# Performance work log

Hardware: AMD Instinct MI355X
Metric: run time of the kernel (lower is better)

The kernel has to match this reference:

```python
import jax, jax.numpy as jnp
import numpy as np


def _maxpool2(x):
    # 2x2 max pool, stride 2, valid padding (H, W even). x: [B,H,W,C]
    B, H, W, C = x.shape
    return x.reshape(B, H // 2, 2, W // 2, 2, C).max(axis=(2, 4))


def setup_inputs() -> dict:
    key = jax.random.key(0)
    ks = jax.random.split(key, 9)
    B, H, W, C = 8, 64, 64, 512
    cfg, ch = C // 8, C // 2
    std = 0.02
    return {
        "x": jax.random.normal(ks[0], (B, H, W, C), jnp.float32),
        "theta_w": jax.random.normal(ks[1], (C, cfg), jnp.float32) * std,
        "theta_b": jnp.zeros((cfg,), jnp.float32),
        "phi_w": jax.random.normal(ks[2], (C, cfg), jnp.float32) * std,
        "phi_b": jnp.zeros((cfg,), jnp.float32),
        "g_w": jax.random.normal(ks[3], (C, ch), jnp.float32) * std,
        "g_b": jnp.zeros((ch,), jnp.float32),
        "o3_w": jax.random.normal(ks[4], (ch, C), jnp.float32) * std,
        "o3_b": jnp.zeros((C,), jnp.float32),
        # original initializes gamma to 0; use 0.1 so the attention branch contributes
        "gamma": jnp.full((1,), 0.1, jnp.float32),
    }


def reference(x, theta_w, theta_b, phi_w, phi_b, g_w, g_b, o3_w, o3_b, gamma):
    B, H, W, C = x.shape
    cfg = theta_w.shape[1]
    ch = g_w.shape[1]
    hw = H * W
    hwd = (H // 2) * (W // 2)

    theta = jnp.einsum("bhwc,cf->bhwf", x, theta_w) + theta_b          # [B,H,W,cfg]
    phi = _maxpool2(jnp.einsum("bhwc,cf->bhwf", x, phi_w) + phi_b)     # [B,H/2,W/2,cfg]
    g = _maxpool2(jnp.einsum("bhwc,cg->bhwg", x, g_w) + g_b)           # [B,H/2,W/2,ch]

    theta_f = theta.reshape(B, hw, cfg)
    phi_f = phi.reshape(B, hwd, cfg)
    g_f = g.reshape(B, hwd, ch)

    # s[b,i,j] = phi[b,i] . theta[b,j]; softmax over j (last axis, Keras default)
    s = jnp.einsum("bif,bjf->bij", phi_f, theta_f)                     # [B,hwd,hw]
    beta = jax.nn.softmax(s, axis=-1)
    # o = matmul(beta, g, transpose_a=True): o[b,j,c] = sum_i beta[b,i,j] g[b,i,c]
    o = jnp.einsum("bij,bic->bjc", beta, g_f)                          # [B,hw,ch]
    o = o.reshape(B, H, W, ch)
    o = jnp.einsum("bhwg,gc->bhwc", o, o3_w) + o3_b                    # [B,H,W,C]
    return gamma * o + x
```

## Files before the change

### kernel.cpp

```cpp
#include <hip/hip_runtime.h>
#include <cstdint>

typedef short short8 __attribute__((ext_vector_type(8)));
typedef float floatx4 __attribute__((ext_vector_type(4)));

__device__ __forceinline__ unsigned short f2bf(float f) {
    unsigned int u = __builtin_bit_cast(unsigned int, f);
    u += 0x7FFFu + ((u >> 16) & 1u);
    return (unsigned short)(u >> 16);
}
__device__ __forceinline__ float bf2f(unsigned short h) {
    unsigned int u = ((unsigned int)h) << 16;
    return __builtin_bit_cast(float, u);
}

__device__ __forceinline__ void async_copy16(const void* g, void* lds) {
    __builtin_amdgcn_global_load_lds(
        (const __attribute__((address_space(1))) void*)g,
        (__attribute__((address_space(3))) void*)lds, 16, 0, 0);
}

template<int EPI>
__global__ __launch_bounds__(256) void mfma_gemm(
    const unsigned short* __restrict__ A, const unsigned short* __restrict__ B,
    void* __restrict__ Cout, const float* __restrict__ bias,
    const float* __restrict__ gamma, const float* __restrict__ resid,
    float* __restrict__ lbuf,
    int lda, int ldb, int ldc, int K,
    long long sA, long long sB, long long sC)
{
    __shared__ unsigned short As[4096];
    __shared__ unsigned short Bs[4096];

    const int tid = threadIdx.x;
    const int wv = tid >> 6, ln = tid & 63;
    const int r16 = ln & 15, q8 = ln >> 4;
    const int wm = (wv >> 1) * 64, wn = (wv & 1) * 64;
    const int m0 = blockIdx.y * 128, n0 = blockIdx.x * 128;
    const int zb = blockIdx.z;

    const unsigned short* Ag = A + (long long)zb * sA;
    const unsigned short* Bg = B + (long long)zb * sB;

    floatx4 acc[4][4] = {};

    for (int k0 = 0; k0 < K; k0 += 32) {
        #pragma unroll
        for (int q = 0; q < 2; ++q) {
            int chunk = wv * 2 + q;
            int e = (chunk << 9) + ln * 8;
            int row = e >> 5, col = e & 31;
            async_copy16(Ag + (size_t)(m0 + row) * lda + (k0 + col), &As[chunk << 9]);
            async_copy16(Bg + (size_t)(n0 + row) * ldb + (k0 + col), &Bs[chunk << 9]);
        }
        __syncthreads();

        short8 af[4], bff[4];
        #pragma unroll
        for (int i = 0; i < 4; ++i) {
            af[i]  = *(const short8*)&As[(wm + i * 16 + r16) * 32 + q8 * 8];
            bff[i] = *(const short8*)&Bs[(wn + i * 16 + r16) * 32 + q8 * 8];
        }
        #pragma unroll
        for (int mi = 0; mi < 4; ++mi)
            #pragma unroll
            for (int ni = 0; ni < 4; ++ni)
                acc[mi][ni] = __builtin_amdgcn_mfma_f32_16x16x32_bf16(
                    af[mi], bff[ni], acc[mi][ni], 0, 0, 0);
        __syncthreads();
    }

    if (EPI == 2) {
        float* C = (float*)Cout;
        const float gm = gamma[0];
        #pragma unroll
        for (int ni = 0; ni < 4; ++ni) {
            const int n = n0 + wn + ni * 16 + r16;
            const float bs = bias[n];
            #pragma unroll
            for (int mi = 0; mi < 4; ++mi)
                #pragma unroll
                for (int r = 0; r < 4; ++r) {
                    int m = m0 + wm + mi * 16 + q8 * 4 + r;
                    C[(size_t)m * ldc + n] = gm * (acc[mi][ni][r] + bs) + resid[(size_t)m * ldc + n];
                }
        }
    } else {
        unsigned short* C = (unsigned short*)Cout + (long long)zb * sC;
        float colsum[4] = {0.f, 0.f, 0.f, 0.f};
        #pragma unroll
        for (int ni = 0; ni < 4; ++ni) {
            const int n = n0 + wn + ni * 16 + r16;
            const float bs = (EPI == 1) ? bias[n] : 0.f;
            #pragma unroll
            for (int mi = 0; mi < 4; ++mi)
                #pragma unroll
                for (int r = 0; r < 4; ++r) {
                    int m = m0 + wm + mi * 16 + q8 * 4 + r;
                    float v = acc[mi][ni][r];
                    if (EPI == 1) v += bs;
                    if (EPI == 3) { v = __expf(v - 20.f); colsum[ni] += v; }
                    C[(size_t)m * ldc + n] = f2bf(v);
                }
        }
        if (EPI == 3) {
            #pragma unroll
            for (int ni = 0; ni < 4; ++ni) {
                float s = colsum[ni];
                s += __shfl_xor(s, 16);
                s += __shfl_xor(s, 32);
                if (q8 == 0)
                    atomicAdd(&lbuf[zb * 1024 + n0 + wn + ni * 16 + r16], s);
            }
        }
    }
}

__global__ __launch_bounds__(256) void prep_w_kernel(
    const float* __restrict__ theta_w, const float* __restrict__ phi_w,
    const float* __restrict__ g_w, const float* __restrict__ o3_w,
    const float* __restrict__ theta_b, const float* __restrict__ phi_b,
    unsigned short* __restrict__ tpwT, unsigned short* __restrict__ gwT,
    unsigned short* __restrict__ o3wT, float* __restrict__ biasTP,
    float* __restrict__ lbuf)
{
    int t = blockIdx.x * 256 + threadIdx.x;
    if (t < 65536) {
        int n = t >> 9, k = t & 511;
        float v = (n < 64) ? theta_w[k * 64 + n] : phi_w[k * 64 + (n - 64)];
        tpwT[t] = f2bf(v);
    } else if (t < 196608) {
        int e = t - 65536; int n = e >> 9, k = e & 511;
        gwT[e] = f2bf(g_w[k * 256 + n]);
    } else if (t < 327680) {
        int e = t - 196608; int n = e >> 8, k = e & 255;
        o3wT[e] = f2bf(o3_w[k * 512 + n]);
    } else if (t < 327808) {
        int j = t - 327680;
        biasTP[j] = (j < 64) ? theta_b[j] : phi_b[j - 64];
    } else if (t < 336000) {
        lbuf[t - 327808] = 0.f;
    }
}

__global__ __launch_bounds__(256) void cast_x_kernel(
    const float* __restrict__ x, unsigned short* __restrict__ xb)
{
    size_t t = (size_t)blockIdx.x * 256 + threadIdx.x;
    float4 v = ((const float4*)x)[t];
    ushort4 h;
    h.x = f2bf(v.x); h.y = f2bf(v.y); h.z = f2bf(v.z); h.w = f2bf(v.w);
    ((ushort4*)xb)[t] = h;
}

__global__ __launch_bounds__(256) void maxpool_phi_kernel(
    const unsigned short* __restrict__ tpF, unsigned short* __restrict__ phiP)
{
    int t = blockIdx.x * 256 + threadIdx.x;
    int f = t & 63, i = (t >> 6) & 1023, b = t >> 16;
    int ph = i >> 5, pw = i & 31;
    size_t base = ((size_t)(b * 64 + 2 * ph) * 64 + 2 * pw) * 128 + 64 + f;
    float v0 = bf2f(tpF[base]),        v1 = bf2f(tpF[base + 128]);
    float v2 = bf2f(tpF[base + 8192]), v3 = bf2f(tpF[base + 8192 + 128]);
    phiP[t] = f2bf(fmaxf(fmaxf(v0, v1), fmaxf(v2, v3)));
}

__global__ __launch_bounds__(256) void maxpoolT_g_kernel(
    const unsigned short* __restrict__ gF, unsigned short* __restrict__ gPT)
{
    __shared__ unsigned short tile[16][256];
    int b = blockIdx.y, i0 = blockIdx.x * 16, c = threadIdx.x;
    #pragma unroll
    for (int il = 0; il < 16; ++il) {
        int i = i0 + il, ph = i >> 5, pw = i & 31;
        size_t base = ((size_t)(b * 64 + 2 * ph) * 64 + 2 * pw) * 256 + c;
        float v0 = bf2f(gF[base]),         v1 = bf2f(gF[base + 256]);
        float v2 = bf2f(gF[base + 16384]), v3 = bf2f(gF[base + 16384 + 256]);
        tile[il][c] = f2bf(fmaxf(fmaxf(v0, v1), fmaxf(v2, v3)));
    }
    __syncthreads();
    unsigned short* dst = gPT + ((size_t)(b * 256 + c) * 1024 + i0);
    short8 v0, v1;
    #pragma unroll
    for (int il = 0; il < 8; ++il) { v0[il] = (short)tile[il][c]; v1[il] = (short)tile[il + 8][c]; }
    *(short8*)dst = v0;
    *(short8*)(dst + 8) = v1;
}

__global__ __launch_bounds__(256) void scale_gpt_kernel(
    unsigned short* __restrict__ gPT, const float* __restrict__ lbuf)
{
    int t = blockIdx.x * 256 + threadIdx.x;
    int i = t & 1023, b = t >> 18;
    float rl = 1.0f / lbuf[b * 1024 + i];
    gPT[t] = f2bf(bf2f(gPT[t]) * rl);
}

extern "C" void kernel_launch(void* const* d_in, const int* in_sizes, int n_in,
                              void* d_out, int out_size, void* d_ws, size_t ws_size,
                              hipStream_t stream)
{
    const float* x       = (const float*)d_in[0];
    const float* theta_w = (const float*)d_in[1];
    const float* theta_b = (const float*)d_in[2];
    const float* phi_w   = (const float*)d_in[3];
    const float* phi_b   = (const float*)d_in[4];
    const float* g_w     = (const float*)d_in[5];
    const float* g_b     = (const float*)d_in[6];
    const float* o3_w    = (const float*)d_in[7];
    const float* o3_b    = (const float*)d_in[8];
    const float* gamma   = (const float*)d_in[9];

    char* ws = (char*)d_ws;
    const size_t MB = 1u << 20;
    unsigned short* tpwT = (unsigned short*)(ws);
    unsigned short* gwT  = (unsigned short*)(ws + 131072);
    unsigned short* o3wT = (unsigned short*)(ws + 393216);
    float* biasTP        = (float*)(ws + 655360);
    float* lbuf          = (float*)(ws + 655872);
    unsigned short* gPT  = (unsigned short*)(ws + 1 * MB);
    unsigned short* tpF  = (unsigned short*)(ws + 5 * MB);
    unsigned short* phiP = (unsigned short*)(ws + 13 * MB);
    unsigned short* gF   = (unsigned short*)(ws + 14 * MB);
    unsigned short* xb   = (unsigned short*)(ws + 30 * MB);
    unsigned short* o_   = (unsigned short*)(ws + 30 * MB);
    unsigned short* sT   = (unsigned short*)d_out;

    prep_w_kernel<<<1313, 256, 0, stream>>>(theta_w, phi_w, g_w, o3_w, theta_b, phi_b,
                                            tpwT, gwT, o3wT, biasTP, lbuf);
    cast_x_kernel<<<16384, 256, 0, stream>>>(x, xb);
    mfma_gemm<1><<<dim3(2, 256, 1), 256, 0, stream>>>(
        xb, gwT, gF, g_b, nullptr, nullptr, nullptr, 512, 512, 256, 512, 0, 0, 0);
    maxpoolT_g_kernel<<<dim3(64, 8), 256, 0, stream>>>(gF, gPT);
    mfma_gemm<1><<<dim3(1, 256, 1), 256, 0, stream>>>(
        xb, tpwT, tpF, biasTP, nullptr, nullptr, nullptr, 512, 512, 128, 512, 0, 0, 0);
    maxpool_phi_kernel<<<2048, 256, 0, stream>>>(tpF, phiP);
    mfma_gemm<3><<<dim3(8, 32, 8), 256, 0, stream>>>(
        tpF, phiP, sT, nullptr, nullptr, nullptr, lbuf,
        128, 64, 1024, 64, 4096LL * 128, 1024LL * 64, 4096LL * 1024);
    scale_gpt_kernel<<<8192, 256, 0, stream>>>(gPT, lbuf);
    mfma_gemm<0><<<dim3(2, 32, 8), 256, 0, stream>>>(
        sT, gPT, o_, nullptr, nullptr, nullptr, nullptr,
        1024, 1024, 256, 1024, 4096LL * 1024, 256LL * 1024, 4096LL * 256);
    mfma_gemm<2><<<dim3(4, 256, 1), 256, 0, stream>>>(
        o_, o3wT, d_out, o3_b, gamma, x, nullptr, 256, 256, 512, 256, 0, 0, 0);
}
```

Measured before the change: 267.4 us.

## Fuse attention score/softmax/PV into one kernel and merge projection GEMMs

Merges the theta/phi/g projections into one GEMM that reads fp32 x directly and converts it to bf16 in-kernel, which removes the separate cast pass. The score GEMM now only accumulates softmax denominators and no longer writes the 4096x1024 score matrix. A new fused kernel recomputes scores per tile, applies exp and normalization, and multiplies by pooled g in LDS. This avoids the large sT round trip through HBM and the scale_gpt pass, at the cost of computing the score GEMM twice and running a fused kernel with heavier LDS use and no async copies.

```diff
diff --git a/kernel.cpp b/kernel.cpp
--- a/kernel.cpp
+++ b/kernel.cpp
@@ -20,9 +20,9 @@
         (__attribute__((address_space(3))) void*)lds, 16, 0, 0);
 }
 
-template<int EPI>
+template<bool AFP32, int EPI>
 __global__ __launch_bounds__(256) void mfma_gemm(
-    const unsigned short* __restrict__ A, const unsigned short* __restrict__ B,
+    const void* __restrict__ Avoid, const unsigned short* __restrict__ B,
     void* __restrict__ Cout, const float* __restrict__ bias,
     const float* __restrict__ gamma, const float* __restrict__ resid,
     float* __restrict__ lbuf,
@@ -39,19 +39,39 @@
     const int m0 = blockIdx.y * 128, n0 = blockIdx.x * 128;
     const int zb = blockIdx.z;
 
-    const unsigned short* Ag = A + (long long)zb * sA;
     const unsigned short* Bg = B + (long long)zb * sB;
 
     floatx4 acc[4][4] = {};
 
     for (int k0 = 0; k0 < K; k0 += 32) {
-        #pragma unroll
-        for (int q = 0; q < 2; ++q) {
-            int chunk = wv * 2 + q;
-            int e = (chunk << 9) + ln * 8;
-            int row = e >> 5, col = e & 31;
-            async_copy16(Ag + (size_t)(m0 + row) * lda + (k0 + col), &As[chunk << 9]);
-            async_copy16(Bg + (size_t)(n0 + row) * ldb + (k0 + col), &Bs[chunk << 9]);
+        if (AFP32) {
+            const float* Af = (const float*)Avoid;
+            #pragma unroll
+            for (int p = 0; p < 4; ++p) {
+                int u = p * 256 + tid;
+                int row = u >> 3, c4 = u & 7;
+                float4 v = *(const float4*)(Af + (size_t)(m0 + row) * lda + k0 + c4 * 4);
+                ushort4 h;
+                h.x = f2bf(v.x); h.y = f2bf(v.y); h.z = f2bf(v.z); h.w = f2bf(v.w);
+                *(ushort4*)&As[row * 32 + c4 * 4] = h;
+            }
+            #pragma unroll
+            for (int q = 0; q < 2; ++q) {
+                int chunk = wv * 2 + q;
+                int e = (chunk << 9) + ln * 8;
+                int row = e >> 5, col = e & 31;
+                async_copy16(Bg + (size_t)(n0 + row) * ldb + (k0 + col), &Bs[chunk << 9]);
+            }
+        } else {
+            const unsigned short* Ag = (const unsigned short*)Avoid + (long long)zb * sA;
+            #pragma unroll
+            for (int q = 0; q < 2; ++q) {
+                int chunk = wv * 2 + q;
+                int e = (chunk << 9) + ln * 8;
+                int row = e >> 5, col = e & 31;
+                async_copy16(Ag + (size_t)(m0 + row) * lda + (k0 + col), &As[chunk << 9]);
+                async_copy16(Bg + (size_t)(n0 + row) * ldb + (k0 + col), &Bs[chunk << 9]);
+            }
         }
         __syncthreads();
 
@@ -85,97 +105,204 @@
                     C[(size_t)m * ldc + n] = gm * (acc[mi][ni][r] + bs) + resid[(size_t)m * ldc + n];
                 }
         }
+    } else if (EPI == 4) {
+        float colsum[4] = {0.f, 0.f, 0.f, 0.f};
+        #pragma unroll
+        for (int ni = 0; ni < 4; ++ni)
+            #pragma unroll
+            for (int mi = 0; mi < 4; ++mi)
+                #pragma unroll
+                for (int r = 0; r < 4; ++r)
+                    colsum[ni] += __expf(acc[mi][ni][r] - 20.f);
+        #pragma unroll
+        for (int ni = 0; ni < 4; ++ni) {
+            float s = colsum[ni];
+            s += __shfl_xor(s, 16);
+            s += __shfl_xor(s, 32);
+            if (q8 == 0)
+                atomicAdd(&lbuf[zb * 1024 + n0 + wn + ni * 16 + r16], s);
+        }
     } else {
         unsigned short* C = (unsigned short*)Cout + (long long)zb * sC;
-        float colsum[4] = {0.f, 0.f, 0.f, 0.f};
         #pragma unroll
         for (int ni = 0; ni < 4; ++ni) {
             const int n = n0 + wn + ni * 16 + r16;
-            const float bs = (EPI == 1) ? bias[n] : 0.f;
+            const float bs = bias[n];
             #pragma unroll
             for (int mi = 0; mi < 4; ++mi)
                 #pragma unroll
                 for (int r = 0; r < 4; ++r) {
                     int m = m0 + wm + mi * 16 + q8 * 4 + r;
-                    float v = acc[mi][ni][r];
-                    if (EPI == 1) v += bs;
-                    if (EPI == 3) { v = __expf(v - 20.f); colsum[ni] += v; }
-                    C[(size_t)m * ldc + n] = f2bf(v);
+                    C[(size_t)m * ldc + n] = f2bf(acc[mi][ni][r] + bs);
                 }
         }
-        if (EPI == 3) {
-            #pragma unroll
-            for (int ni = 0; ni < 4; ++ni) {
-                float s = colsum[ni];
-                s += __shfl_xor(s, 16);
-                s += __shfl_xor(s, 32);
-                if (q8 == 0)
-                    atomicAdd(&lbuf[zb * 1024 + n0 + wn + ni * 16 + r16], s);
+    }
+}
+
+__global__ __launch_bounds__(256) void attn_fused_kernel(
+    const unsigned short* __restrict__ tpgF,
+    const unsigned short* __restrict__ phiP,
+    const unsigned short* __restrict__ gPT,
+    const float* __restrict__ lbuf,
+    unsigned short* __restrict__ o_)
+{
+    __shared__ unsigned short th_s[128 * 72];
+    __shared__ unsigned short ph_s[64 * 72];
+    __shared__ unsigned short es[128 * 72];
+    __shared__ unsigned short gs[128 * 72];
+    __shared__ float rl_s[1024];
+
+    const int tid = threadIdx.x, wv = tid >> 6, ln = tid & 63;
+    const int r16 = ln & 15, q8 = ln >> 4;
+    const int c0 = blockIdx.x * 128, j0 = blockIdx.y * 128, b = blockIdx.z;
+    const int wm = (wv >> 1) * 64, wn = (wv & 1) * 64;
+
+    {
+        const unsigned short* src = tpgF + (size_t)(b * 4096 + j0) * 384;
+        #pragma unroll
+        for (int p = 0; p < 4; ++p) {
+            int u = p * 256 + tid;
+            int row = u >> 3, cu = u & 7;
+            *(short8*)&th_s[row * 72 + cu * 8] =
+                *(const short8*)(src + (size_t)row * 384 + cu * 8);
+        }
+        #pragma unroll
+        for (int p = 0; p < 4; ++p) {
+            int i = p * 256 + tid;
+            rl_s[i] = 1.0f / lbuf[b * 1024 + i];
+        }
+    }
+
+    floatx4 acc[4][4] = {};
+
+    for (int i0 = 0; i0 < 1024; i0 += 64) {
+        #pragma unroll
+        for (int p = 0; p < 2; ++p) {
+            int u = p * 256 + tid;
+            int row = u >> 3, cu = u & 7;
+            *(short8*)&ph_s[row * 72 + cu * 8] =
+                *(const short8*)(phiP + ((size_t)b * 1024 + i0 + row) * 64 + cu * 8);
+        }
+        #pragma unroll
+        for (int p = 0; p < 4; ++p) {
+            int u = p * 256 + tid;
+            int row = u >> 3, cu = u & 7;
+            *(short8*)&gs[row * 72 + cu * 8] =
+                *(const short8*)(gPT + ((size_t)(b * 256 + c0 + row)) * 1024 + i0 + cu * 8);
+        }
+        __syncthreads();
+
+        floatx4 sacc[2][4] = {};
+        #pragma unroll
+        for (int ks = 0; ks < 2; ++ks) {
+            short8 saf[2], sbf[4];
+            #pragma unroll
+            for (int mi = 0; mi < 2; ++mi)
+                saf[mi] = *(const short8*)&th_s[(wv * 32 + mi * 16 + r16) * 72 + ks * 32 + q8 * 8];
+            #pragma unroll
+            for (int ni = 0; ni < 4; ++ni)
+                sbf[ni] = *(const short8*)&ph_s[(ni * 16 + r16) * 72 + ks * 32 + q8 * 8];
+            #pragma unroll
+            for (int mi = 0; mi < 2; ++mi)
+                #pragma unroll
+                for (int ni = 0; ni < 4; ++ni)
+                    sacc[mi][ni] = __builtin_amdgcn_mfma_f32_16x16x32_bf16(
+                        saf[mi], sbf[ni], sacc[mi][ni], 0, 0, 0);
+        }
+        #pragma unroll
+        for (int ni = 0; ni < 4; ++ni) {
+            float rl = rl_s[i0 + ni * 16 + r16];
+            #pragma unroll
+            for (int mi = 0; mi < 2; ++mi)
+                #pragma unroll
+                for (int r = 0; r < 4; ++r) {
+                    int jl = wv * 32 + mi * 16 + q8 * 4 + r;
+                    int il = ni * 16 + r16;
+                    es[jl * 72 + il] = f2bf(__expf(sacc[mi][ni][r] - 20.f) * rl);
+                }
+        }
+        __syncthreads();
+
+        #pragma unroll
+        for (int ks = 0; ks < 2; ++ks) {
+            short8 oaf[4], obf[4];
+            #pragma unroll
+            for (int mi = 0; mi < 4; ++mi)
+                oaf[mi] = *(const short8*)&es[(wm + mi * 16 + r16) * 72 + ks * 32 + q8 * 8];
+            #pragma unroll
+            for (int ni = 0; ni < 4; ++ni)
+                obf[ni] = *(const short8*)&gs[(wn + ni * 16 + r16) * 72 + ks * 32 + q8 * 8];
+            #pragma unroll
+            for (int mi = 0; mi < 4; ++mi)
+                #pragma unroll
+                for (int ni = 0; ni < 4; ++ni)
+                    acc[mi][ni] = __builtin_amdgcn_mfma_f32_16x16x32_bf16(
+                        oaf[mi], obf[ni], acc[mi][ni], 0, 0, 0);
+        }
+        __syncthreads();
+    }
+
+    #pragma unroll
+    for (int ni = 0; ni < 4; ++ni)
+        #pragma unroll
+        for (int mi = 0; mi < 4; ++mi)
+            #pragma unroll
+            for (int r = 0; r < 4; ++r) {
+                int j = j0 + wm + mi * 16 + q8 * 4 + r;
+                int c = c0 + wn + ni * 16 + r16;
+                o_[((size_t)b * 4096 + j) * 256 + c] = f2bf(acc[mi][ni][r]);
             }
-        }
-    }
 }
 
 __global__ __launch_bounds__(256) void prep_w_kernel(
     const float* __restrict__ theta_w, const float* __restrict__ phi_w,
     const float* __restrict__ g_w, const float* __restrict__ o3_w,
     const float* __restrict__ theta_b, const float* __restrict__ phi_b,
-    unsigned short* __restrict__ tpwT, unsigned short* __restrict__ gwT,
-    unsigned short* __restrict__ o3wT, float* __restrict__ biasTP,
-    float* __restrict__ lbuf)
+    const float* __restrict__ g_b,
+    unsigned short* __restrict__ tpgwT, unsigned short* __restrict__ o3wT,
+    float* __restrict__ biasTPG, float* __restrict__ lbuf)
 {
     int t = blockIdx.x * 256 + threadIdx.x;
-    if (t < 65536) {
+    if (t < 196608) {
         int n = t >> 9, k = t & 511;
-        float v = (n < 64) ? theta_w[k * 64 + n] : phi_w[k * 64 + (n - 64)];
-        tpwT[t] = f2bf(v);
-    } else if (t < 196608) {
-        int e = t - 65536; int n = e >> 9, k = e & 511;
-        gwT[e] = f2bf(g_w[k * 256 + n]);
+        float v = (n < 64) ? theta_w[k * 64 + n]
+                : (n < 128) ? phi_w[k * 64 + (n - 64)]
+                : g_w[k * 256 + (n - 128)];
+        tpgwT[t] = f2bf(v);
     } else if (t < 327680) {
         int e = t - 196608; int n = e >> 8, k = e & 255;
         o3wT[e] = f2bf(o3_w[k * 512 + n]);
-    } else if (t < 327808) {
+    } else if (t < 328064) {
         int j = t - 327680;
-        biasTP[j] = (j < 64) ? theta_b[j] : phi_b[j - 64];
-    } else if (t < 336000) {
-        lbuf[t - 327808] = 0.f;
-    }
-}
-
-__global__ __launch_bounds__(256) void cast_x_kernel(
-    const float* __restrict__ x, unsigned short* __restrict__ xb)
-{
-    size_t t = (size_t)blockIdx.x * 256 + threadIdx.x;
-    float4 v = ((const float4*)x)[t];
-    ushort4 h;
-    h.x = f2bf(v.x); h.y = f2bf(v.y); h.z = f2bf(v.z); h.w = f2bf(v.w);
-    ((ushort4*)xb)[t] = h;
+        biasTPG[j] = (j < 64) ? theta_b[j] : (j < 128) ? phi_b[j - 64] : g_b[j - 128];
+    } else if (t < 336256) {
+        lbuf[t - 328064] = 0.f;
+    }
 }
 
 __global__ __launch_bounds__(256) void maxpool_phi_kernel(
-    const unsigned short* __restrict__ tpF, unsigned short* __restrict__ phiP)
+    const unsigned short* __restrict__ tpgF, unsigned short* __restrict__ phiP)
 {
     int t = blockIdx.x * 256 + threadIdx.x;
     int f = t & 63, i = (t >> 6) & 1023, b = t >> 16;
     int ph = i >> 5, pw = i & 31;
-    size_t base = ((size_t)(b * 64 + 2 * ph) * 64 + 2 * pw) * 128 + 64 + f;
-    float v0 = bf2f(tpF[base]),        v1 = bf2f(tpF[base + 128]);
-    float v2 = bf2f(tpF[base + 8192]), v3 = bf2f(tpF[base + 8192 + 128]);
+    size_t base = ((size_t)(b * 64 + 2 * ph) * 64 + 2 * pw) * 384 + 64 + f;
+    float v0 = bf2f(tpgF[base]),         v1 = bf2f(tpgF[base + 384]);
+    float v2 = bf2f(tpgF[base + 24576]), v3 = bf2f(tpgF[base + 24576 + 384]);
     phiP[t] = f2bf(fmaxf(fmaxf(v0, v1), fmaxf(v2, v3)));
 }
 
 __global__ __launch_bounds__(256) void maxpoolT_g_kernel(
-    const unsigned short* __restrict__ gF, unsigned short* __restrict__ gPT)
+    const unsigned short* __restrict__ tpgF, unsigned short* __restrict__ gPT)
 {
     __shared__ unsigned short tile[16][256];
     int b = blockIdx.y, i0 = blockIdx.x * 16, c = threadIdx.x;
     #pragma unroll
     for (int il = 0; il < 16; ++il) {
         int i = i0 + il, ph = i >> 5, pw = i & 31;
-        size_t base = ((size_t)(b * 64 + 2 * ph) * 64 + 2 * pw) * 256 + c;
-        float v0 = bf2f(gF[base]),         v1 = bf2f(gF[base + 256]);
-        float v2 = bf2f(gF[base + 16384]), v3 = bf2f(gF[base + 16384 + 256]);
+        size_t base = ((size_t)(b * 64 + 2 * ph) * 64 + 2 * pw) * 384 + 128 + c;
+        float v0 = bf2f(tpgF[base]),         v1 = bf2f(tpgF[base + 384]);
+        float v2 = bf2f(tpgF[base + 24576]), v3 = bf2f(tpgF[base + 24576 + 384]);
         tile[il][c] = f2bf(fmaxf(fmaxf(v0, v1), fmaxf(v2, v3)));
     }
     __syncthreads();
@@ -185,15 +312,6 @@
     for (int il = 0; il < 8; ++il) { v0[il] = (short)tile[il][c]; v1[il] = (short)tile[il + 8][c]; }
     *(short8*)dst = v0;
     *(short8*)(dst + 8) = v1;
-}
-
-__global__ __launch_bounds__(256) void scale_gpt_kernel(
-    unsigned short* __restrict__ gPT, const float* __restrict__ lbuf)
-{
-    int t = blockIdx.x * 256 + threadIdx.x;
-    int i = t & 1023, b = t >> 18;
-    float rl = 1.0f / lbuf[b * 1024 + i];
-    gPT[t] = f2bf(bf2f(gPT[t]) * rl);
 }
 
 extern "C" void kernel_launch(void* const* d_in, const int* in_sizes, int n_in,
@@ -212,36 +330,28 @@
     const float* gamma   = (const float*)d_in[9];
 
     char* ws = (char*)d_ws;
-    const size_t MB = 1u << 20;
-    unsigned short* tpwT = (unsigned short*)(ws);
-    unsigned short* gwT  = (unsigned short*)(ws + 131072);
-    unsigned short* o3wT = (unsigned short*)(ws + 393216);
-    float* biasTP        = (float*)(ws + 655360);
-    float* lbuf          = (float*)(ws + 655872);
-    unsigned short* gPT  = (unsigned short*)(ws + 1 * MB);
-    unsigned short* tpF  = (unsigned short*)(ws + 5 * MB);
-    unsigned short* phiP = (unsigned short*)(ws + 13 * MB);
-    unsigned short* gF   = (unsigned short*)(ws + 14 * MB);
-    unsigned short* xb   = (unsigned short*)(ws + 30 * MB);
-    unsigned short* o_   = (unsigned short*)(ws + 30 * MB);
-    unsigned short* sT   = (unsigned short*)d_out;
-
-    prep_w_kernel<<<1313, 256, 0, stream>>>(theta_w, phi_w, g_w, o3_w, theta_b, phi_b,
-                                            tpwT, gwT, o3wT, biasTP, lbuf);
-    cast_x_kernel<<<16384, 256, 0, stream>>>(x, xb);
-    mfma_gemm<1><<<dim3(2, 256, 1), 256, 0, stream>>>(
-        xb, gwT, gF, g_b, nullptr, nullptr, nullptr, 512, 512, 256, 512, 0, 0, 0);
-    maxpoolT_g_kernel<<<dim3(64, 8), 256, 0, stream>>>(gF, gPT);
-    mfma_gemm<1><<<dim3(1, 256, 1), 256, 0, stream>>>(
-        xb, tpwT, tpF, biasTP, nullptr, nullptr, nullptr, 512, 512, 128, 512, 0, 0, 0);
-    maxpool_phi_kernel<<<2048, 256, 0, stream>>>(tpF, phiP);
-    mfma_gemm<3><<<dim3(8, 32, 8), 256, 0, stream>>>(
-        tpF, phiP, sT, nullptr, nullptr, nullptr, lbuf,
-        128, 64, 1024, 64, 4096LL * 128, 1024LL * 64, 4096LL * 1024);
-    scale_gpt_kernel<<<8192, 256, 0, stream>>>(gPT, lbuf);
-    mfma_gemm<0><<<dim3(2, 32, 8), 256, 0, stream>>>(
-        sT, gPT, o_, nullptr, nullptr, nullptr, nullptr,
-        1024, 1024, 256, 1024, 4096LL * 1024, 256LL * 1024, 4096LL * 256);
-    mfma_gemm<2><<<dim3(4, 256, 1), 256, 0, stream>>>(
-        o_, o3wT, d_out, o3_b, gamma, x, nullptr, 256, 256, 512, 256, 0, 0, 0);
-}
+    unsigned short* tpgwT  = (unsigned short*)(ws);
+    unsigned short* o3wT   = (unsigned short*)(ws + 393216);
+    float* biasTPG         = (float*)(ws + 655360);
+    float* lbuf            = (float*)(ws + 656896);
+    unsigned short* tpgF   = (unsigned short*)(ws + (1u << 20));
+    unsigned short* phiP   = (unsigned short*)(ws + (1u << 20) + 25165824);
+    unsigned short* gPT    = (unsigned short*)(ws + (1u << 20) + 26214400);
+    unsigned short* o_     = (unsigned short*)(ws + (1u << 20) + 30408704);
+
+    prep_w_kernel<<<1314, 256, 0, stream>>>(theta_w, phi_w, g_w, o3_w,
+                                            theta_b, phi_b, g_b,
+                                            tpgwT, o3wT, biasTPG, lbuf);
+    mfma_gemm<true, 1><<<dim3(3, 256, 1), 256, 0, stream>>>(
+        x, tpgwT, tpgF, biasTPG, nullptr, nullptr, nullptr,
+        512, 512, 384, 512, 0, 0, 0);
+    maxpool_phi_kernel<<<2048, 256, 0, stream>>>(tpgF, phiP);
+    maxpoolT_g_kernel<<<dim3(64, 8), 256, 0, stream>>>(tpgF, gPT);
+    mfma_gemm<false, 4><<<dim3(8, 32, 8), 256, 0, stream>>>(
+        tpgF, phiP, nullptr, nullptr, nullptr, nullptr, lbuf,
+        384, 64, 0, 64, 4096LL * 384, 1024LL * 64, 0);
+    attn_fused_kernel<<<dim3(2, 32, 8), 256, 0, stream>>>(tpgF, phiP, gPT, lbuf, o_);
+    mfma_gemm<false, 2><<<dim3(4, 256, 1), 256, 0, stream>>>(
+        o_, o3wT, d_out, o3_b, gamma, x, nullptr,
+        256, 256, 512, 256, 0, 0, 0);
+}
```

Result: faster. 252.8 us (-5.5%).
